# Kernel tuning notes

Hardware: AMD Instinct MI355X
Metric: run time of the kernel (lower is better)

## Reference

```python
import jax, jax.numpy as jnp
import numpy as np


def setup_inputs() -> dict:
    key = jax.random.key(0)
    k1, k2, k3, k4, k5 = jax.random.split(key, 5)
    B, C, H, W = 4, 256, 64, 64
    d = C // 2  # red = 2
    s = 1.0 / np.sqrt(C)
    so = 1.0 / np.sqrt(d)
    return {
        "x": jax.random.normal(k1, (B, C, H, W), dtype=jnp.float32),
        "w_theta": jax.random.normal(k2, (d, C), dtype=jnp.float32) * s,
        "w_phi": jax.random.normal(k3, (d, C), dtype=jnp.float32) * s,
        "w_g": jax.random.normal(k4, (d, C), dtype=jnp.float32) * s,
        "w_out": jax.random.normal(k5, (C, d), dtype=jnp.float32) * so,
    }


def reference(x, w_theta, w_phi, w_g, w_out):
    B, C, H, W = x.shape
    N = H * W
    xf = x.reshape(B, C, N)  # [B, C, N]
    # 1x1 convs (bias-free) are per-pixel channel matmuls
    th = jnp.einsum("dc,bcn->bdn", w_theta, xf)  # [B, d, N]
    ph = jnp.einsum("dc,bcn->bdn", w_phi, xf)    # [B, d, N]
    g = jnp.einsum("dc,bcn->bdn", w_g, xf)       # [B, d, N]
    # attn[b, n, m] = softmax_m( th[b,:,n] . ph[b,:,m] )  (unscaled, embedded Gaussian)
    scores = jnp.einsum("bdn,bdm->bnm", th, ph)  # [B, N, N]
    attn = jax.nn.softmax(scores, axis=-1)
    # y = bmm(g, attn^T): y[b,d,n] = sum_m g[b,d,m] * attn[b,n,m]
    y = jnp.einsum("bdm,bnm->bdn", g, attn)      # [B, d, N]
    out = jnp.einsum("cd,bdn->bcn", w_out, y)    # [B, C, N]
    return x + out.reshape(B, C, H, W)
```

## Files before the change

### kernel.cpp

```cpp
#include <hip/hip_runtime.h>

#define B_ 4
#define C_ 256
#define D_ 128
#define N_ 4096
#define LOG2E 1.44269504088896340736f
#define M_FIX 90.0f

typedef __attribute__((ext_vector_type(8))) short short8_t;
typedef __attribute__((ext_vector_type(4))) short short4_t;
typedef __attribute__((ext_vector_type(4))) float f32x4;
typedef _Float16 half8_t __attribute__((ext_vector_type(8)));
typedef _Float16 half4_t __attribute__((ext_vector_type(4)));

__device__ __forceinline__ unsigned short f2bf(float f) {
    union { float f; unsigned int u; } c; c.f = f;
    unsigned int r = (c.u + 0x7fffu + ((c.u >> 16) & 1u)) >> 16;
    return (unsigned short)r;
}
__device__ __forceinline__ float bf2f(unsigned int u) {
    union { unsigned int u; float f; } c; c.u = (u & 0xffffu) << 16;
    return c.f;
}
__device__ __forceinline__ unsigned short f2h(float f) {
    union { _Float16 h; unsigned short u; } c; c.h = (_Float16)f;
    return c.u;
}
__device__ __forceinline__ unsigned int cvtpk_bf16(float lo, float hi) {
    unsigned int r;
    asm("v_cvt_pk_bf16_f32 %0, %1, %2" : "=v"(r) : "v"(lo), "v"(hi));
    return r;
}

#define GLOAD16(gp, lp)                                                     \
    __builtin_amdgcn_global_load_lds(                                       \
        (const __attribute__((address_space(1))) unsigned int*)(gp),        \
        (__attribute__((address_space(3))) unsigned int*)(lp), 16, 0, 0)

__global__ __launch_bounds__(256) void wcvt_kernel(
    const float* __restrict__ w_theta, const float* __restrict__ w_phi,
    const float* __restrict__ w_g, const float* __restrict__ w_out,
    unsigned short* __restrict__ wF, unsigned short* __restrict__ woutF)
{
    int tid = blockIdx.x * 256 + threadIdx.x;
    if (tid < 3 * 32768) {
        int wi = tid >> 15, off = tid & 32767;
        const float* src = (wi == 0) ? w_theta : (wi == 1) ? w_phi : w_g;
        float v = src[off] * ((wi == 0) ? LOG2E : 1.f);
        wF[tid] = f2h(v);
    } else {
        int off = tid - 3 * 32768;
        woutF[off] = f2bf(w_out[off]);
    }
}

__global__ __launch_bounds__(256) void proj_mfma(
    const float* __restrict__ x, const unsigned short* __restrict__ wF,
    unsigned short* __restrict__ Qf, unsigned short* __restrict__ Kf,
    unsigned short* __restrict__ Vt)
{
    const int n0 = blockIdx.x * 32;
    const int b  = blockIdx.y;

    __shared__ _Float16 xs[256 * 36];

    const int t  = threadIdx.x;
    const int w  = t >> 6;
    const int l  = t & 63;
    const int lr = l & 15;
    const int lg = l >> 4;

    const float* xb = x + (size_t)b * C_ * N_;
    {
        const int cb = t >> 3, n2 = t & 7;
        #pragma unroll
        for (int p = 0; p < 8; ++p) {
            const int c = 32 * p + cb;
            float4 v = *reinterpret_cast<const float4*>(&xb[(size_t)c * N_ + n0 + 4 * n2]);
            union { _Float16 h[4]; uint2 u; } pk;
            pk.h[0] = (_Float16)v.x; pk.h[1] = (_Float16)v.y;
            pk.h[2] = (_Float16)v.z; pk.h[3] = (_Float16)v.w;
            *reinterpret_cast<uint2*>(&xs[c * 36 + 4 * n2]) = pk.u;
        }
    }
    __syncthreads();

    f32x4 acc[6][2];
    #pragma unroll
    for (int d = 0; d < 6; ++d)
        #pragma unroll
        for (int nt = 0; nt < 2; ++nt) acc[d][nt] = (f32x4){0.f, 0.f, 0.f, 0.f};

    #pragma unroll
    for (int kt = 0; kt < 8; ++kt) {
        half8_t xf[2];
        #pragma unroll
        for (int nt = 0; nt < 2; ++nt)
            #pragma unroll
            for (int j = 0; j < 8; ++j)
                xf[nt][j] = xs[(32 * kt + 8 * lg + j) * 36 + 16 * nt + lr];
        #pragma unroll
        for (int d = 0; d < 6; ++d) {
            const int gt = 6 * w + d;
            half8_t wf = *reinterpret_cast<const half8_t*>(
                &wF[(size_t)(16 * gt + lr) * 256 + 32 * kt + 8 * lg]);
            if (gt < 16) {
                #pragma unroll
                for (int nt = 0; nt < 2; ++nt)
                    acc[d][nt] = __builtin_amdgcn_mfma_f32_16x16x32_f16(wf, xf[nt], acc[d][nt], 0, 0, 0);
            } else {
                #pragma unroll
                for (int nt = 0; nt < 2; ++nt)
                    acc[d][nt] = __builtin_amdgcn_mfma_f32_16x16x32_f16(xf[nt], wf, acc[d][nt], 0, 0, 0);
            }
        }
    }

    #pragma unroll
    for (int d = 0; d < 6; ++d) {
        const int gt = 6 * w + d;
        #pragma unroll
        for (int nt = 0; nt < 2; ++nt) {
            if (gt < 16) {
                unsigned short* o = (gt < 8) ? Qf : Kf;
                half4_t s;
                #pragma unroll
                for (int r = 0; r < 4; ++r) s[r] = (_Float16)acc[d][nt][r];
                size_t idx = ((size_t)(b * N_ + n0 + 16 * nt + lr)) * D_ + (gt & 7) * 16 + 4 * lg;
                *reinterpret_cast<half4_t*>(&o[idx]) = s;
            } else {
                short4_t s;
                #pragma unroll
                for (int r = 0; r < 4; ++r) s[r] = (short)f2bf(acc[d][nt][r]);
                size_t idx = ((size_t)b * D_ + (gt - 16) * 16 + lr) * N_ + n0 + 16 * nt + 4 * lg;
                *reinterpret_cast<short4_t*>(&Vt[idx]) = s;
            }
        }
    }
}

__global__ __launch_bounds__(512, 4) void flash_mfma(
    const unsigned short* __restrict__ Qg,
    const unsigned short* __restrict__ Kg,
    const unsigned short* __restrict__ Vg,
    unsigned short* __restrict__ Yp, float* __restrict__ Lg)
{
    const int id    = blockIdx.x;
    const int local = id >> 3;
    const int group = (id & 7) * 2 + (local >> 5);
    const int qblk  = local & 31;
    const int h     = group & 3;
    const int b     = group >> 2;
    const int q0    = qblk * 128;
    const int m_base = h * 1024;

    __shared__ unsigned short Ks[2][64 * 128];
    __shared__ unsigned short Vs[2][128 * 64];

    const int t  = threadIdx.x;
    const int w  = t >> 6;
    const int l  = t & 63;
    const int lr = l & 15;
    const int lg = l >> 4;

    half8_t qf[4];
    {
        const unsigned short* qp =
            Qg + ((size_t)(b * N_ + q0 + w * 16 + lr)) * D_ + lg * 8;
        #pragma unroll
        for (int kt = 0; kt < 4; ++kt)
            qf[kt] = *reinterpret_cast<const half8_t*>(qp + 32 * kt);
    }

    f32x4 Yf[8];
    #pragma unroll
    for (int i = 0; i < 8; ++i) Yf[i] = (f32x4){0.f, 0.f, 0.f, 0.f};
    f32x4 lacc = (f32x4){0.f, 0.f, 0.f, 0.f};

    short8_t ones;
    #pragma unroll
    for (int i = 0; i < 8; ++i) ones[i] = (short)0x3F80;

    const unsigned short* Kbp = Kg + (size_t)b * N_ * D_;
    const unsigned short* Vbp = Vg + (size_t)b * D_ * N_;
    const int krow0 = 8 * w + (l >> 4);
    const int krow1 = krow0 + 4;
    const unsigned short* kp0 = Kbp + (size_t)(m_base + krow0) * D_ + (((l & 15) ^ (krow0 & 15)) * 8);
    const unsigned short* kp1 = Kbp + (size_t)(m_base + krow1) * D_ + (((l & 15) ^ (krow1 & 15)) * 8);
    const int vrow0 = 16 * w + (l >> 3);
    const int vrow1 = vrow0 + 8;
    const unsigned short* vp0 = Vbp + (size_t)vrow0 * N_ + m_base + (((l & 7) ^ (vrow0 & 7)) * 8);
    const unsigned short* vp1 = Vbp + (size_t)vrow1 * N_ + m_base + (((l & 7) ^ (vrow1 & 7)) * 8);

    GLOAD16(kp0, &Ks[0][(8 * w) * 128]);
    GLOAD16(kp1, &Ks[0][(8 * w + 4) * 128]);
    GLOAD16(vp0, &Vs[0][(16 * w) * 64]);
    GLOAD16(vp1, &Vs[0][(16 * w + 8) * 64]);
    __syncthreads();

    for (int it = 0; it < 16; ++it) {
        const int cur = it & 1;
        if (it + 1 < 16) {
            const size_t ko = (size_t)(it + 1) * 8192;
            const size_t vo = (size_t)(it + 1) * 64;
            GLOAD16(kp0 + ko, &Ks[cur ^ 1][(8 * w) * 128]);
            GLOAD16(kp1 + ko, &Ks[cur ^ 1][(8 * w + 4) * 128]);
            GLOAD16(vp0 + vo, &Vs[cur ^ 1][(16 * w) * 64]);
            GLOAD16(vp1 + vo, &Vs[cur ^ 1][(16 * w + 8) * 64]);
        }

        f32x4 S[4];
        #pragma unroll
        for (int mt = 0; mt < 4; ++mt)
            S[mt] = (f32x4){-M_FIX, -M_FIX, -M_FIX, -M_FIX};
        __builtin_amdgcn_s_setprio(1);
        #pragma unroll
        for (int kt = 0; kt < 4; ++kt) {
            #pragma unroll
            for (int mt = 0; mt < 4; ++mt) {
                const int row = lr + 16 * mt;
                const int off = row * 128 + (((lg + 4 * kt) ^ lr) * 8);
                half8_t kf = *reinterpret_cast<const half8_t*>(&Ks[cur][off]);
                S[mt] = __builtin_amdgcn_mfma_f32_16x16x32_f16(kf, qf[kt], S[mt], 0, 0, 0);
            }
        }
        __builtin_amdgcn_s_setprio(0);

        #pragma unroll
        for (int mt = 0; mt < 4; ++mt)
            #pragma unroll
            for (int r = 0; r < 4; ++r)
                S[mt][r] = exp2f(S[mt][r]);
        unsigned int pk[4][2];
        #pragma unroll
        for (int mt = 0; mt < 4; ++mt) {
            pk[mt][0] = cvtpk_bf16(S[mt][0], S[mt][1]);
            pk[mt][1] = cvtpk_bf16(S[mt][2], S[mt][3]);
        }

        __builtin_amdgcn_s_setprio(1);
        #pragma unroll
        for (int mk = 0; mk < 2; ++mk) {
            short8_t pb;
            unsigned int* pbw = reinterpret_cast<unsigned int*>(&pb);
            #pragma unroll
            for (int wd = 0; wd < 4; ++wd) {
                int src = lr + 16 * (2 * (lg & 1) + (wd >> 1));
                unsigned int vA = __shfl(pk[2 * mk][wd & 1], src, 64);
                unsigned int vB = __shfl(pk[2 * mk + 1][wd & 1], src, 64);
                pbw[wd] = (lg >> 1) ? vB : vA;
            }
            #pragma unroll
            for (int dt = 0; dt < 8; ++dt) {
                const int row = lr + 16 * dt;
                const int voff = row * 64 + (((lg + 4 * mk) ^ (lr & 7)) * 8);
                short8_t vf = *reinterpret_cast<const short8_t*>(&Vs[cur][voff]);
                Yf[dt] = __builtin_amdgcn_mfma_f32_16x16x32_bf16(vf, pb, Yf[dt], 0, 0, 0);
            }
            lacc = __builtin_amdgcn_mfma_f32_16x16x32_bf16(ones, pb, lacc, 0, 0, 0);
        }
        __builtin_amdgcn_s_setprio(0);

        __syncthreads();
    }

    const int q = q0 + w * 16 + lr;
    const size_t ybase = ((size_t)(h * B_ + b) * N_ + q) * D_;
    #pragma unroll
    for (int dt = 0; dt < 8; ++dt) {
        short4_t s;
        #pragma unroll
        for (int r = 0; r < 4; ++r) s[r] = (short)f2bf(Yf[dt][r]);
        *reinterpret_cast<short4_t*>(&Yp[ybase + 16 * dt + lg * 4]) = s;
    }
    if (lg == 0)
        Lg[(size_t)(h * B_ + b) * N_ + q] = lacc[0];
}

__global__ __launch_bounds__(256) void flash_merge(
    const unsigned short* __restrict__ Yp, const float* __restrict__ Lg,
    unsigned short* __restrict__ Yg)
{
    int idx = blockIdx.x * 256 + threadIdx.x;
    int dd2 = (idx & 63) * 2;
    int n   = (idx >> 6) & (N_ - 1);
    int b   = idx >> 18;
    float lsum = 0.f, a0 = 0.f, a1 = 0.f;
    #pragma unroll
    for (int h = 0; h < 4; ++h) {
        lsum += Lg[(size_t)(h * B_ + b) * N_ + n];
        unsigned int u = *reinterpret_cast<const unsigned int*>(
            &Yp[((size_t)(h * B_ + b) * N_ + n) * D_ + dd2]);
        a0 += bf2f(u);
        a1 += bf2f(u >> 16);
    }
    float inv = 1.f / lsum;
    unsigned int o = (unsigned int)f2bf(a0 * inv) | ((unsigned int)f2bf(a1 * inv) << 16);
    *reinterpret_cast<unsigned int*>(&Yg[((size_t)b * N_ + n) * D_ + dd2]) = o;
}

__global__ __launch_bounds__(256) void out_mfma(
    const float* __restrict__ x, const unsigned short* __restrict__ woutF,
    const unsigned short* __restrict__ Y, float* __restrict__ out)
{
    const int n0 = blockIdx.x * 64;
    const int cy = blockIdx.y;
    const int b  = blockIdx.z;

    const int t  = threadIdx.x;
    const int w  = t >> 6;
    const int l  = t & 63;
    const int lr = l & 15;
    const int lg = l >> 4;

    f32x4 acc[2][4];
    #pragma unroll
    for (int ci = 0; ci < 2; ++ci)
        #pragma unroll
        for (int nt = 0; nt < 4; ++nt) acc[ci][nt] = (f32x4){0.f, 0.f, 0.f, 0.f};

    const unsigned short* Yb = Y + (size_t)b * N_ * D_;
    #pragma unroll
    for (int kt = 0; kt < 4; ++kt) {
        short8_t yf[4];
        #pragma unroll
        for (int nt = 0; nt < 4; ++nt)
            yf[nt] = *reinterpret_cast<const short8_t*>(
                &Yb[(size_t)(n0 + 16 * nt + lr) * D_ + 32 * kt + 8 * lg]);
        #pragma unroll
        for (int ci = 0; ci < 2; ++ci) {
            const int c = cy * 128 + (2 * w + ci) * 16 + lr;
            short8_t wf = *reinterpret_cast<const short8_t*>(
                &woutF[(size_t)c * D_ + 32 * kt + 8 * lg]);
            #pragma unroll
            for (int nt = 0; nt < 4; ++nt)
                acc[ci][nt] = __builtin_amdgcn_mfma_f32_16x16x32_bf16(yf[nt], wf, acc[ci][nt], 0, 0, 0);
        }
    }

    #pragma unroll
    for (int ci = 0; ci < 2; ++ci) {
        const int c = cy * 128 + (2 * w + ci) * 16 + lr;
        #pragma unroll
        for (int nt = 0; nt < 4; ++nt) {
            size_t idx = ((size_t)b * C_ + c) * N_ + n0 + 16 * nt + 4 * lg;
            float4 xv = *reinterpret_cast<const float4*>(&x[idx]);
            *reinterpret_cast<float4*>(&out[idx]) =
                make_float4(acc[ci][nt][0] + xv.x, acc[ci][nt][1] + xv.y,
                            acc[ci][nt][2] + xv.z, acc[ci][nt][3] + xv.w);
        }
    }
}

extern "C" void kernel_launch(void* const* d_in, const int* in_sizes, int n_in,
                              void* d_out, int out_size, void* d_ws, size_t ws_size,
                              hipStream_t stream)
{
    const float* x       = (const float*)d_in[0];
    const float* w_theta = (const float*)d_in[1];
    const float* w_phi   = (const float*)d_in[2];
    const float* w_g     = (const float*)d_in[3];
    const float* w_out   = (const float*)d_in[4];
    float* outp = (float*)d_out;

    const size_t nq = (size_t)B_ * N_ * D_;
    unsigned short* Qf    = (unsigned short*)d_ws;
    unsigned short* Kf    = Qf + nq;
    unsigned short* Vt    = Kf + nq;
    float*          Lg    = (float*)(Vt + nq);
    unsigned short* wF    = (unsigned short*)(Lg + 4 * B_ * N_);
    unsigned short* woutF = wF + 3 * 128 * 256;
    unsigned short* Yp    = (unsigned short*)d_out;
    unsigned short* Y     = Kf;

    wcvt_kernel<<<dim3(512), 256, 0, stream>>>(w_theta, w_phi, w_g, w_out, wF, woutF);
    proj_mfma<<<dim3(N_ / 32, B_), 256, 0, stream>>>(x, wF, Qf, Kf, Vt);
    flash_mfma<<<dim3(512), 512, 0, stream>>>(Qf, Kf, Vt, Yp, Lg);
    flash_merge<<<dim3((B_ * N_ * (D_ / 2)) / 256), 256, 0, stream>>>(Yp, Lg, Y);
    out_mfma<<<dim3(N_ / 64, 2, B_), 256, 0, stream>>>(x, woutF, Y, outp);
}
```

Measured before the change: 96.92 us.

## Load V fragments directly from global into registers, dropping LDS staging

Removes the double-buffered V shared-memory tiles and their async global-to-LDS copies. Each lane now reads its V MFMA operands straight from global memory into registers during each iteration, interleaved with the softmax and P shuffles. This halves LDS use and removes LDS reads for V, which may raise occupancy. The cost is that every wave now issues its own uncoalesced-ish global loads for the same V data, which used to be shared across the 8 waves. Latency is no longer hidden by prefetch one tile ahead, and register pressure grows by 16 short8 values.

```diff
diff --git a/kernel.cpp b/kernel.cpp
--- a/kernel.cpp
+++ b/kernel.cpp
@@ -155,7 +155,6 @@
     const int m_base = h * 1024;
 
     __shared__ unsigned short Ks[2][64 * 128];
-    __shared__ unsigned short Vs[2][128 * 64];
 
     const int t  = threadIdx.x;
     const int w  = t >> 6;
@@ -182,31 +181,24 @@
     for (int i = 0; i < 8; ++i) ones[i] = (short)0x3F80;
 
     const unsigned short* Kbp = Kg + (size_t)b * N_ * D_;
-    const unsigned short* Vbp = Vg + (size_t)b * D_ * N_;
     const int krow0 = 8 * w + (l >> 4);
     const int krow1 = krow0 + 4;
     const unsigned short* kp0 = Kbp + (size_t)(m_base + krow0) * D_ + (((l & 15) ^ (krow0 & 15)) * 8);
     const unsigned short* kp1 = Kbp + (size_t)(m_base + krow1) * D_ + (((l & 15) ^ (krow1 & 15)) * 8);
-    const int vrow0 = 16 * w + (l >> 3);
-    const int vrow1 = vrow0 + 8;
-    const unsigned short* vp0 = Vbp + (size_t)vrow0 * N_ + m_base + (((l & 7) ^ (vrow0 & 7)) * 8);
-    const unsigned short* vp1 = Vbp + (size_t)vrow1 * N_ + m_base + (((l & 7) ^ (vrow1 & 7)) * 8);
+
+    const unsigned short* vlane =
+        Vg + (size_t)b * D_ * N_ + (size_t)lr * N_ + m_base + 8 * lg;
 
     GLOAD16(kp0, &Ks[0][(8 * w) * 128]);
     GLOAD16(kp1, &Ks[0][(8 * w + 4) * 128]);
-    GLOAD16(vp0, &Vs[0][(16 * w) * 64]);
-    GLOAD16(vp1, &Vs[0][(16 * w + 8) * 64]);
     __syncthreads();
 
     for (int it = 0; it < 16; ++it) {
         const int cur = it & 1;
         if (it + 1 < 16) {
             const size_t ko = (size_t)(it + 1) * 8192;
-            const size_t vo = (size_t)(it + 1) * 64;
             GLOAD16(kp0 + ko, &Ks[cur ^ 1][(8 * w) * 128]);
             GLOAD16(kp1 + ko, &Ks[cur ^ 1][(8 * w + 4) * 128]);
-            GLOAD16(vp0 + vo, &Vs[cur ^ 1][(16 * w) * 64]);
-            GLOAD16(vp1 + vo, &Vs[cur ^ 1][(16 * w + 8) * 64]);
         }
 
         f32x4 S[4];
@@ -226,6 +218,12 @@
         }
         __builtin_amdgcn_s_setprio(0);
 
+        const unsigned short* vit = vlane + it * 64;
+        short8_t vr0[8];
+        #pragma unroll
+        for (int dt = 0; dt < 8; ++dt)
+            vr0[dt] = *reinterpret_cast<const short8_t*>(vit + (size_t)dt * 16 * N_);
+
         #pragma unroll
         for (int mt = 0; mt < 4; ++mt)
             #pragma unroll
@@ -238,27 +236,47 @@
             pk[mt][1] = cvtpk_bf16(S[mt][2], S[mt][3]);
         }
 
-        __builtin_amdgcn_s_setprio(1);
-        #pragma unroll
-        for (int mk = 0; mk < 2; ++mk) {
-            short8_t pb;
-            unsigned int* pbw = reinterpret_cast<unsigned int*>(&pb);
+        short8_t pb0;
+        {
+            unsigned int* pbw = reinterpret_cast<unsigned int*>(&pb0);
             #pragma unroll
             for (int wd = 0; wd < 4; ++wd) {
                 int src = lr + 16 * (2 * (lg & 1) + (wd >> 1));
-                unsigned int vA = __shfl(pk[2 * mk][wd & 1], src, 64);
-                unsigned int vB = __shfl(pk[2 * mk + 1][wd & 1], src, 64);
+                unsigned int vA = __shfl(pk[0][wd & 1], src, 64);
+                unsigned int vB = __shfl(pk[1][wd & 1], src, 64);
                 pbw[wd] = (lg >> 1) ? vB : vA;
             }
-            #pragma unroll
-            for (int dt = 0; dt < 8; ++dt) {
-                const int row = lr + 16 * dt;
-                const int voff = row * 64 + (((lg + 4 * mk) ^ (lr & 7)) * 8);
-                short8_t vf = *reinterpret_cast<const short8_t*>(&Vs[cur][voff]);
-                Yf[dt] = __builtin_amdgcn_mfma_f32_16x16x32_bf16(vf, pb, Yf[dt], 0, 0, 0);
-            }
-            lacc = __builtin_amdgcn_mfma_f32_16x16x32_bf16(ones, pb, lacc, 0, 0, 0);
-        }
+        }
+
+        short8_t vr1[8];
+        #pragma unroll
+        for (int dt = 0; dt < 8; ++dt)
+            vr1[dt] = *reinterpret_cast<const short8_t*>(vit + (size_t)dt * 16 * N_ + 32);
+
+        __builtin_amdgcn_s_setprio(1);
+        #pragma unroll
+        for (int dt = 0; dt < 8; ++dt)
+            Yf[dt] = __builtin_amdgcn_mfma_f32_16x16x32_bf16(vr0[dt], pb0, Yf[dt], 0, 0, 0);
+        lacc = __builtin_amdgcn_mfma_f32_16x16x32_bf16(ones, pb0, lacc, 0, 0, 0);
+        __builtin_amdgcn_s_setprio(0);
+
+        short8_t pb1;
+        {
+            unsigned int* pbw = reinterpret_cast<unsigned int*>(&pb1);
+            #pragma unroll
+            for (int wd = 0; wd < 4; ++wd) {
+                int src = lr + 16 * (2 * (lg & 1) + (wd >> 1));
+                unsigned int vA = __shfl(pk[2][wd & 1], src, 64);
+                unsigned int vB = __shfl(pk[3][wd & 1], src, 64);
+                pbw[wd] = (lg >> 1) ? vB : vA;
+            }
+        }
+
+        __builtin_amdgcn_s_setprio(1);
+        #pragma unroll
+        for (int dt = 0; dt < 8; ++dt)
+            Yf[dt] = __builtin_amdgcn_mfma_f32_16x16x32_bf16(vr1[dt], pb1, Yf[dt], 0, 0, 0);
+        lacc = __builtin_amdgcn_mfma_f32_16x16x32_bf16(ones, pb1, lacc, 0, 0, 0);
         __builtin_amdgcn_s_setprio(0);
 
         __syncthreads();
```

Result: slower. 237.3 us (+144.8%).
